# Optimization experiments

Hardware: AMD Instinct MI355X
Metric: run time of the kernel (lower is better)

## Reference

```python
import jax, jax.numpy as jnp
import numpy as np

B, S, IN_DIM = 8, 4096, 1024
H, D = 16, 64          # num_heads, head_dim (attention_dim = H*D = 1024)
OUT_DIM = 1024
EPS = 1e-6
HI = jax.lax.Precision.HIGHEST


def setup_inputs() -> dict:
    key = jax.random.key(0)
    ks = jax.random.split(key, 9)
    sx = 1.0 / np.sqrt(IN_DIM)
    so = 1.0 / np.sqrt(H * D)
    return {
        "x":  jax.random.normal(ks[0], (B, S, IN_DIM), jnp.float32),
        "wq": jax.random.normal(ks[1], (IN_DIM, H, D), jnp.float32) * sx,
        "bq": jnp.zeros((H, D), jnp.float32),
        "wk": jax.random.normal(ks[2], (IN_DIM, H, D), jnp.float32) * sx,
        "bk": jnp.zeros((H, D), jnp.float32),
        "wv": jax.random.normal(ks[3], (IN_DIM, H, D), jnp.float32) * sx,
        "bv": jnp.zeros((H, D), jnp.float32),
        "wo": jax.random.normal(ks[4], (H, D, OUT_DIM), jnp.float32) * so,
        "bo": jnp.zeros((OUT_DIM,), jnp.float32),
    }


def _feature_map(t):
    return jax.nn.elu(t) + 1.0


def reference(x, wq, bq, wk, bk, wv, bv, wo, bo):
    # QKV projections: [B,S,IN] x [IN,H,D] -> [B,S,H,D]
    q = jnp.einsum('bsi,ihd->bshd', x, wq) + bq
    k = jnp.einsum('bsi,ihd->bshd', x, wk) + bk
    v = jnp.einsum('bsi,ihd->bshd', x, wv) + bv

    Q = _feature_map(q)
    K = _feature_map(k)

    # Faithful to source: KV is an elementwise K*V reduced over seq -> [B,H,D]
    KV = jnp.einsum('bshd,bshd->bhd', K, v, precision=HI)
    Ksum = jnp.sum(K, axis=1)                      # [B,H,D]
    Z = 1.0 / (Q * Ksum[:, None, :, :] + EPS)      # [B,S,H,D]
    attn = Q * KV[:, None, :, :] * Z               # [B,S,H,D]

    # output projection contracts heads and head_dim
    out = jnp.einsum('bshd,hdo->bso', attn, wo) + bo
    return jax.nn.gelu(out)  # flax default gelu is approximate=True
```

## Files before the change

kernel.cpp:

```cpp
#include <hip/hip_runtime.h>


#define SEQ   4096
#define MROWS 32768
#define KDIM  1024
#define HD    1024
#define T32   32

typedef __bf16 bf16x8 __attribute__((ext_vector_type(8)));
typedef float floatx4 __attribute__((ext_vector_type(4)));

__device__ __forceinline__ unsigned short f2bf(float f) {
    unsigned int u = __float_as_uint(f);
    u += 0x7fffu + ((u >> 16) & 1u);
    return (unsigned short)(u >> 16);
}
__device__ __forceinline__ void cvt8(const float* __restrict__ p, unsigned short* d) {
    const float4 a = *(const float4*)p;
    const float4 b = *(const float4*)(p + 4);
    d[0] = f2bf(a.x); d[1] = f2bf(a.y); d[2] = f2bf(a.z); d[3] = f2bf(a.w);
    d[4] = f2bf(b.x); d[5] = f2bf(b.y); d[6] = f2bf(b.z); d[7] = f2bf(b.w);
}

typedef const __attribute__((address_space(1))) unsigned int* gas_t;
typedef __attribute__((address_space(3))) unsigned int* las_t;
__device__ __forceinline__ void async16(const void* g, void* l) {
    __builtin_amdgcn_global_load_lds((gas_t)g, (las_t)l, 16, 0, 0);
}

__global__ __launch_bounds__(256)
void prep(const float* __restrict__ x, unsigned short* __restrict__ xb,
          const float* __restrict__ wk, const float* __restrict__ wv,
          unsigned short* __restrict__ wkT, unsigned short* __restrict__ wvT,
          float4* __restrict__ KVZ4)
{
    __shared__ alignas(16) unsigned short Ts[64][72];
    const int t = threadIdx.x;
    if (blockIdx.x < 16384) {
        const size_t p = ((size_t)blockIdx.x * 256 + t) * 8;
        union { uint4 u; unsigned short s[8]; } o;
        cvt8(x + p, o.s);
        *(uint4*)(xb + p) = o.u;
        return;
    }
    if (blockIdx.x >= 16384 + 512) {
#pragma unroll
        for (int i = 0; i < 16; ++i)
            KVZ4[t * 16 + i] = (float4){0.f, 0.f, 0.f, 0.f};
        return;
    }
    const int bid = blockIdx.x - 16384;
    const float* W = (bid >> 8) ? wv : wk;
    unsigned short* WT = (bid >> 8) ? wvT : wkT;
    const int k0 = (bid & 15) * 64, n0 = ((bid >> 4) & 15) * 64;
    const int r4 = (t >> 4) * 4, c4 = (t & 15) * 4;
#pragma unroll
    for (int i = 0; i < 4; i++) {
        const float4 f = *(const float4*)(W + (size_t)(k0 + r4 + i) * HD + n0 + c4);
        Ts[c4 + 0][r4 + i] = f2bf(f.x);
        Ts[c4 + 1][r4 + i] = f2bf(f.y);
        Ts[c4 + 2][r4 + i] = f2bf(f.z);
        Ts[c4 + 3][r4 + i] = f2bf(f.w);
    }
    __syncthreads();
    const int rr = t >> 3, cc = (t & 7) * 8;
#pragma unroll
    for (int h = 0; h < 2; h++)
        *(uint4*)(WT + (size_t)(n0 + rr + h * 32) * KDIM + k0 + cc) =
            *(const uint4*)&Ts[rr + h * 32][cc];
}

__global__ __launch_bounds__(512, 1)
void kv_gemm_fast(const unsigned short* __restrict__ xb,
                  const unsigned short* __restrict__ wkT,
                  const unsigned short* __restrict__ wvT,
                  const float* __restrict__ bk, const float* __restrict__ bv,
                  float2* __restrict__ KVZ)
{
    __shared__ alignas(16) unsigned short As[4][256 * 32];
    __shared__ alignas(16) unsigned short Bs[4][256 * 32];

    const int t = threadIdx.x;

    const int id = blockIdx.x;
    const int xcd = id & 7, o = id >> 3;
    const int mtile = xcd * 16 + (o >> 3);
    const int ntile = o & 7;
    const int m0 = mtile * 256;
    const int n0 = ntile * 128;
    const int b  = m0 >> 12;

    const int w = t >> 6, lane = t & 63;
    const int wm = w >> 1, wn = w & 1;
    const int lrow = lane & 15, quad = lane >> 4;

    const int usw = quad ^ ((lrow >> 1) & 3);

    const int srow  = t >> 2;
    const int usrc  = (t & 3) ^ ((t >> 3) & 3);
    const unsigned short* gA0 = xb  + (size_t)(m0 + srow) * KDIM + usrc * 8;
    const unsigned short* gA1 = gA0 + (size_t)128 * KDIM;
    const unsigned short* gBk = wkT + (size_t)(n0 + srow) * KDIM + usrc * 8;
    const unsigned short* gBv = wvT + (size_t)(n0 + srow) * KDIM + usrc * 8;

#define STAGE(c, tk) do {                                                     \
        const int ko_ = (tk) * 32;                                            \
        async16(gA0 + ko_, &As[c][(0 * 512 + t) * 8]);                        \
        async16(gA1 + ko_, &As[c][(1 * 512 + t) * 8]);                        \
        async16(gBk + ko_, &Bs[c][(0 * 512 + t) * 8]);                        \
        async16(gBv + ko_, &Bs[c][(1 * 512 + t) * 8]);                        \
    } while (0)

    STAGE(0, 0);
    STAGE(1, 1);
    STAGE(2, 2);

    floatx4 accK[4][4], accV[4][4];
#pragma unroll
    for (int i = 0; i < 4; i++)
#pragma unroll
        for (int j = 0; j < 4; j++) {
            accK[i][j] = (floatx4){0.f, 0.f, 0.f, 0.f};
            accV[i][j] = (floatx4){0.f, 0.f, 0.f, 0.f};
        }

    asm volatile("s_waitcnt vmcnt(8)" ::: "memory");
    __builtin_amdgcn_s_barrier();

    for (int tk = 0; tk < T32; ++tk) {
        const unsigned short* A = As[tk & 3];
        const unsigned short* B = Bs[tk & 3];

        bf16x8 af[4], bK[4], bV[4];
#pragma unroll
        for (int mi = 0; mi < 4; ++mi)
            af[mi] = *(const bf16x8*)&A[(wm * 64 + mi * 16 + lrow) * 32 + usw * 8];
#pragma unroll
        for (int ni = 0; ni < 4; ++ni) {
            const int br = wn * 64 + ni * 16 + lrow;
            bK[ni] = *(const bf16x8*)&B[ br        * 32 + usw * 8];
            bV[ni] = *(const bf16x8*)&B[(br + 128) * 32 + usw * 8];
        }

        __builtin_amdgcn_s_setprio(1);
#pragma unroll
        for (int mi = 0; mi < 4; ++mi)
#pragma unroll
            for (int ni = 0; ni < 4; ++ni) {
                accK[mi][ni] = __builtin_amdgcn_mfma_f32_16x16x32_bf16(
                    af[mi], bK[ni], accK[mi][ni], 0, 0, 0);
                accV[mi][ni] = __builtin_amdgcn_mfma_f32_16x16x32_bf16(
                    af[mi], bV[ni], accV[mi][ni], 0, 0, 0);
            }
        __builtin_amdgcn_s_setprio(0);

        if (tk + 3 < T32) {
            STAGE((tk + 3) & 3, tk + 3);
            asm volatile("s_waitcnt vmcnt(8)" ::: "memory");
        } else if (tk == T32 - 3) {
            asm volatile("s_waitcnt vmcnt(4)" ::: "memory");
        } else if (tk == T32 - 2) {
            asm volatile("s_waitcnt vmcnt(0)" ::: "memory");
        }
        __builtin_amdgcn_s_barrier();
    }
#undef STAGE

#pragma unroll
    for (int ni = 0; ni < 4; ++ni) {
        const int colw = n0 + wn * 64 + ni * 16 + lrow;
        const float bkf = bk[colw];
        const float bvf = bv[colw];
        float pKV = 0.f, pK = 0.f;
#pragma unroll
        for (int mi = 0; mi < 4; ++mi) {
#pragma unroll
            for (int r = 0; r < 4; ++r) {
                const float kk = accK[mi][ni][r] + bkf;
                const float K  = (kk > 0.f) ? (kk + 1.f) : __expf(kk);
                const float vv = accV[mi][ni][r] + bvf;
                pKV += K * vv;
                pK  += K;
            }
        }
        pKV += __shfl_xor(pKV, 16, 64);
        pKV += __shfl_xor(pKV, 32, 64);
        pK  += __shfl_xor(pK, 16, 64);
        pK  += __shfl_xor(pK, 32, 64);
        if (quad == 0) {
            atomicAdd(&KVZ[b * HD + colw].x, pKV);
            atomicAdd(&KVZ[b * HD + colw].y, pK);
        }
    }
}

__global__ __launch_bounds__(256)
void kv_gemm(const float* __restrict__ x,
             const float* __restrict__ wk, const float* __restrict__ bk,
             const float* __restrict__ wv, const float* __restrict__ bv,
             float2* __restrict__ KVZ)
{
    __shared__ alignas(16) unsigned short As [128][40];
    __shared__ alignas(16) unsigned short BsK[128][40];
    __shared__ alignas(16) unsigned short BsV[128][40];

    const int t = threadIdx.x;
    const int n0 = blockIdx.x * 128;
    const int m0 = blockIdx.y * 128;
    const int b  = m0 >> 12;

    const int wave = t >> 6, lane = t & 63;
    const int wm = wave >> 1, wn = wave & 1;
    const int lrow = lane & 15, quad = lane >> 4;

    floatx4 accK[4][4], accV[4][4];
#pragma unroll
    for (int i = 0; i < 4; i++)
#pragma unroll
        for (int j = 0; j < 4; j++) {
            accK[i][j] = (floatx4){0.f, 0.f, 0.f, 0.f};
            accV[i][j] = (floatx4){0.f, 0.f, 0.f, 0.f};
        }

    const int arow0 = t >> 2, akc = (t & 3) * 8;
    const int bk0 = t >> 4, bnc = (t & 15) * 8;

    for (int k0 = 0; k0 < KDIM; k0 += 32) {
        __syncthreads();
        {
            union { uint4 u; unsigned short s[8]; } ua, ub;
            cvt8(x + (size_t)(m0 + arow0) * KDIM + k0 + akc, ua.s);
            cvt8(x + (size_t)(m0 + arow0 + 64) * KDIM + k0 + akc, ub.s);
            *(uint4*)&As[arow0][akc] = ua.u;
            *(uint4*)&As[arow0 + 64][akc] = ub.u;
        }
        {
            unsigned short k0s[8], k1s[8], v0s[8], v1s[8];
            cvt8(wk + (size_t)(k0 + bk0) * HD + n0 + bnc, k0s);
            cvt8(wk + (size_t)(k0 + bk0 + 16) * HD + n0 + bnc, k1s);
            cvt8(wv + (size_t)(k0 + bk0) * HD + n0 + bnc, v0s);
            cvt8(wv + (size_t)(k0 + bk0 + 16) * HD + n0 + bnc, v1s);
#pragma unroll
            for (int j = 0; j < 8; j++) {
                BsK[bnc + j][bk0]      = k0s[j];
                BsK[bnc + j][bk0 + 16] = k1s[j];
                BsV[bnc + j][bk0]      = v0s[j];
                BsV[bnc + j][bk0 + 16] = v1s[j];
            }
        }
        __syncthreads();

        bf16x8 af[4], bfK[4], bfV[4];
#pragma unroll
        for (int mi = 0; mi < 4; mi++)
            af[mi] = *(const bf16x8*)&As[wm * 64 + mi * 16 + lrow][quad * 8];
#pragma unroll
        for (int ni = 0; ni < 4; ni++) {
            bfK[ni] = *(const bf16x8*)&BsK[wn * 64 + ni * 16 + lrow][quad * 8];
            bfV[ni] = *(const bf16x8*)&BsV[wn * 64 + ni * 16 + lrow][quad * 8];
        }
#pragma unroll
        for (int mi = 0; mi < 4; mi++)
#pragma unroll
            for (int ni = 0; ni < 4; ni++) {
                accK[mi][ni] = __builtin_amdgcn_mfma_f32_16x16x32_bf16(
                    af[mi], bfK[ni], accK[mi][ni], 0, 0, 0);
                accV[mi][ni] = __builtin_amdgcn_mfma_f32_16x16x32_bf16(
                    af[mi], bfV[ni], accV[mi][ni], 0, 0, 0);
            }
    }

#pragma unroll
    for (int ni = 0; ni < 4; ni++) {
        const int colw = n0 + wn * 64 + ni * 16 + lrow;
        const float bkf = bk[colw];
        const float bvf = bv[colw];
        float pKV = 0.f, pK = 0.f;
#pragma unroll
        for (int mi = 0; mi < 4; mi++) {
#pragma unroll
            for (int r = 0; r < 4; r++) {
                const float kk = accK[mi][ni][r] + bkf;
                const float K  = (kk > 0.f) ? (kk + 1.f) : __expf(kk);
                const float vv = accV[mi][ni][r] + bvf;
                pKV += K * vv;
                pK  += K;
            }
        }
        pKV += __shfl_xor(pKV, 16, 64);
        pKV += __shfl_xor(pKV, 32, 64);
        pK  += __shfl_xor(pK, 16, 64);
        pK  += __shfl_xor(pK, 32, 64);
        if (quad == 0) {
            atomicAdd(&KVZ[b * HD + colw].x, pKV);
            atomicAdd(&KVZ[b * HD + colw].y, pK);
        }
    }
}

__global__ __launch_bounds__(256)
void rowgemm_bcast(const float2* __restrict__ KVZ,
                   const float* __restrict__ wo, const float* __restrict__ bo,
                   float* __restrict__ out)
{
    __shared__ float a[1024];
    __shared__ float red[4][64];
    __shared__ float sval[64];
    const int t = threadIdx.x;
    const int b = blockIdx.x;
    const int o0 = blockIdx.y * 64;
    const int s0 = blockIdx.z * 512;

    for (int c = t; c < 1024; c += 256) {
        const float2 z = KVZ[b * HD + c];
        a[c] = z.x / z.y;
    }
    __syncthreads();

    const int cs = t >> 6, oi = t & 63;
    float p = 0.f;
    const int cbeg = cs * 256;
    for (int c = cbeg; c < cbeg + 256; ++c)
        p += a[c] * wo[(size_t)c * HD + o0 + oi];
    red[cs][oi] = p;
    __syncthreads();

    if (t < 64) {
        float v = red[0][t] + red[1][t] + red[2][t] + red[3][t] + bo[o0 + t];
        sval[t] = 0.5f * v *
            (1.f + tanhf(0.7978845608028654f * (v + 0.044715f * v * v * v)));
    }
    __syncthreads();

    const float4 sv4 = *(const float4*)&sval[(t & 15) * 4];
    for (int r = t >> 4; r < 512; r += 16)
        *(float4*)&out[((size_t)(b * SEQ + s0 + r)) * HD + o0 + (t & 15) * 4] = sv4;
}

__global__ __launch_bounds__(256)
void rowgemm(const float2* __restrict__ KVZ,
             const float* __restrict__ wo, const float* __restrict__ bo,
             float* __restrict__ rowf)
{
    __shared__ float a[1024];
    __shared__ float red[4][64];
    const int t = threadIdx.x;
    const int b = blockIdx.x;
    const int o0 = blockIdx.y * 64;

    for (int c = t; c < 1024; c += 256) {
        const float2 z = KVZ[b * HD + c];
        a[c] = z.x / z.y;
    }
    __syncthreads();

    const int cs = t >> 6, oi = t & 63;
    float p = 0.f;
    const int cbeg = cs * 256;
    for (int c = cbeg; c < cbeg + 256; ++c)
        p += a[c] * wo[(size_t)c * HD + o0 + oi];
    red[cs][oi] = p;
    __syncthreads();

    if (t < 64) {
        float v = red[0][t] + red[1][t] + red[2][t] + red[3][t] + bo[o0 + t];
        const float g = 0.5f * v *
            (1.f + tanhf(0.7978845608028654f * (v + 0.044715f * v * v * v)));
        rowf[b * HD + o0 + t] = g;
    }
}

__global__ __launch_bounds__(256)
void broadcast_rows(const float* __restrict__ rowf, float* __restrict__ out)
{
    const size_t idx = (size_t)blockIdx.x * 256 + threadIdx.x;
    const size_t p = idx * 4;
    const int row = (int)(p >> 10);
    const int b = row >> 12;
    const int col = (int)(p & 1023);
    *(float4*)(out + p) = *(const float4*)(rowf + b * HD + col);
}

extern "C" void kernel_launch(void* const* d_in, const int* in_sizes, int n_in,
                              void* d_out, int out_size, void* d_ws, size_t ws_size,
                              hipStream_t stream)
{
    const float* x  = (const float*)d_in[0];
    const float* wk = (const float*)d_in[3];
    const float* bk = (const float*)d_in[4];
    const float* wv = (const float*)d_in[5];
    const float* bv = (const float*)d_in[6];
    const float* wo = (const float*)d_in[7];
    const float* bo = (const float*)d_in[8];
    float* out = (float*)d_out;

    const size_t NEED = (size_t)72 * 1024 * 1024;
    if (ws_size >= NEED) {
        unsigned short* xb  = (unsigned short*)d_ws;
        unsigned short* wkT = (unsigned short*)((char*)d_ws + (67u << 20));
        unsigned short* wvT = (unsigned short*)((char*)d_ws + (69u << 20));
        float2* KVZ = (float2*)((char*)d_ws + (71u << 20));

        prep<<<dim3(16384 + 512 + 1), 256, 0, stream>>>(x, xb, wk, wv, wkT, wvT,
                                                        (float4*)KVZ);
        kv_gemm_fast<<<dim3(1024), 512, 0, stream>>>(xb, wkT, wvT, bk, bv, KVZ);
        rowgemm_bcast<<<dim3(8, 16, 8), 256, 0, stream>>>(KVZ, wo, bo, out);
    } else {
        float2* KVZ = (float2*)d_ws;
        float* rowf = (float*)((char*)d_ws + 65536);
        hipMemsetAsync(KVZ, 0, 8 * HD * sizeof(float2), stream);
        kv_gemm<<<dim3(8, 256), 256, 0, stream>>>(x, wk, bk, wv, bv, KVZ);
        rowgemm<<<dim3(8, 16), 256, 0, stream>>>(KVZ, wo, bo, rowf);
        broadcast_rows<<<dim3((MROWS * HD / 4) / 256), 256, 0, stream>>>(rowf, out);
    }
}
```

Before: 400.0 us.

## Restructure KV-projection GEMM main loop into ping-pong phases with split staging

Rewrites the K/V projection GEMM main loop as an unrolled-by-two schedule that splits each k-step into separate K and V MFMA phases, each bracketed by barriers. A and B tile loads are issued in separate halves between phases, and the last k-steps are peeled into an explicit epilogue. The aim is to interleave global prefetch, LDS reads and MFMA bursts across waves, in the style of a ping-pong schedule. It adds many more barriers per k-step, which could cost more in synchronisation than the overlap gains.

```diff
diff --git a/kernel.cpp b/kernel.cpp
--- a/kernel.cpp
+++ b/kernel.cpp
@@ -5,7 +5,6 @@
 #define MROWS 32768
 #define KDIM  1024
 #define HD    1024
-#define T32   32
 
 typedef __bf16 bf16x8 __attribute__((ext_vector_type(8)));
 typedef float floatx4 __attribute__((ext_vector_type(4)));
@@ -103,17 +102,46 @@
     const unsigned short* gBk = wkT + (size_t)(n0 + srow) * KDIM + usrc * 8;
     const unsigned short* gBv = wvT + (size_t)(n0 + srow) * KDIM + usrc * 8;
 
-#define STAGE(c, tk) do {                                                     \
+#define STAGE_A(c, tk) do {                                                   \
         const int ko_ = (tk) * 32;                                            \
         async16(gA0 + ko_, &As[c][(0 * 512 + t) * 8]);                        \
         async16(gA1 + ko_, &As[c][(1 * 512 + t) * 8]);                        \
+    } while (0)
+#define STAGE_B(c, tk) do {                                                   \
+        const int ko_ = (tk) * 32;                                            \
         async16(gBk + ko_, &Bs[c][(0 * 512 + t) * 8]);                        \
         async16(gBv + ko_, &Bs[c][(1 * 512 + t) * 8]);                        \
     } while (0)
-
-    STAGE(0, 0);
-    STAGE(1, 1);
-    STAGE(2, 2);
+#define READ_AF(Ap_) do { _Pragma("unroll")                                   \
+        for (int mi = 0; mi < 4; ++mi)                                        \
+            af[mi] = *(const bf16x8*)&Ap_[(wm * 64 + mi * 16 + lrow) * 32 + usw * 8]; \
+    } while (0)
+#define READ_BK(Bp_) do { _Pragma("unroll")                                   \
+        for (int ni = 0; ni < 4; ++ni)                                        \
+            bK[ni] = *(const bf16x8*)&Bp_[(wn * 64 + ni * 16 + lrow) * 32 + usw * 8]; \
+    } while (0)
+#define READ_BV(Bp_) do { _Pragma("unroll")                                   \
+        for (int ni = 0; ni < 4; ++ni)                                        \
+            bV[ni] = *(const bf16x8*)&Bp_[(128 + wn * 64 + ni * 16 + lrow) * 32 + usw * 8]; \
+    } while (0)
+#define MFMA_K do { __builtin_amdgcn_s_setprio(1); _Pragma("unroll")          \
+        for (int mi = 0; mi < 4; ++mi) _Pragma("unroll")                      \
+            for (int ni = 0; ni < 4; ++ni)                                    \
+                accK[mi][ni] = __builtin_amdgcn_mfma_f32_16x16x32_bf16(       \
+                    af[mi], bK[ni], accK[mi][ni], 0, 0, 0);                   \
+        __builtin_amdgcn_s_setprio(0); } while (0)
+#define MFMA_V do { __builtin_amdgcn_s_setprio(1); _Pragma("unroll")          \
+        for (int mi = 0; mi < 4; ++mi) _Pragma("unroll")                      \
+            for (int ni = 0; ni < 4; ++ni)                                    \
+                accV[mi][ni] = __builtin_amdgcn_mfma_f32_16x16x32_bf16(       \
+                    af[mi], bV[ni], accV[mi][ni], 0, 0, 0);                   \
+        __builtin_amdgcn_s_setprio(0); } while (0)
+#define BAR   __builtin_amdgcn_s_barrier()
+#define VM(n) asm volatile("s_waitcnt vmcnt(" #n ")" ::: "memory")
+
+    STAGE_A(0, 0); STAGE_B(0, 0);
+    STAGE_A(1, 1); STAGE_B(1, 1);
+    STAGE_A(2, 2); STAGE_B(2, 2);
 
     floatx4 accK[4][4], accV[4][4];
 #pragma unroll
@@ -124,47 +152,76 @@
             accV[i][j] = (floatx4){0.f, 0.f, 0.f, 0.f};
         }
 
-    asm volatile("s_waitcnt vmcnt(8)" ::: "memory");
-    __builtin_amdgcn_s_barrier();
-
-    for (int tk = 0; tk < T32; ++tk) {
-        const unsigned short* A = As[tk & 3];
-        const unsigned short* B = Bs[tk & 3];
-
-        bf16x8 af[4], bK[4], bV[4];
-#pragma unroll
-        for (int mi = 0; mi < 4; ++mi)
-            af[mi] = *(const bf16x8*)&A[(wm * 64 + mi * 16 + lrow) * 32 + usw * 8];
-#pragma unroll
-        for (int ni = 0; ni < 4; ++ni) {
-            const int br = wn * 64 + ni * 16 + lrow;
-            bK[ni] = *(const bf16x8*)&B[ br        * 32 + usw * 8];
-            bV[ni] = *(const bf16x8*)&B[(br + 128) * 32 + usw * 8];
-        }
-
-        __builtin_amdgcn_s_setprio(1);
-#pragma unroll
-        for (int mi = 0; mi < 4; ++mi)
-#pragma unroll
-            for (int ni = 0; ni < 4; ++ni) {
-                accK[mi][ni] = __builtin_amdgcn_mfma_f32_16x16x32_bf16(
-                    af[mi], bK[ni], accK[mi][ni], 0, 0, 0);
-                accV[mi][ni] = __builtin_amdgcn_mfma_f32_16x16x32_bf16(
-                    af[mi], bV[ni], accV[mi][ni], 0, 0, 0);
-            }
-        __builtin_amdgcn_s_setprio(0);
-
-        if (tk + 3 < T32) {
-            STAGE((tk + 3) & 3, tk + 3);
-            asm volatile("s_waitcnt vmcnt(8)" ::: "memory");
-        } else if (tk == T32 - 3) {
-            asm volatile("s_waitcnt vmcnt(4)" ::: "memory");
-        } else if (tk == T32 - 2) {
-            asm volatile("s_waitcnt vmcnt(0)" ::: "memory");
-        }
-        __builtin_amdgcn_s_barrier();
-    }
-#undef STAGE
+    VM(8);
+    BAR;
+
+    bf16x8 af[4], bK[4], bV[4];
+
+    for (int it = 0; it < 14; ++it) {
+        const int tk = it * 2;
+        const unsigned short* A0 = As[tk & 3];
+        const unsigned short* B0 = Bs[tk & 3];
+        const unsigned short* A1 = As[(tk + 1) & 3];
+        const unsigned short* B1 = Bs[(tk + 1) & 3];
+
+        READ_AF(A0); READ_BK(B0);
+        STAGE_A((tk + 3) & 3, tk + 3);
+        BAR; MFMA_K; BAR;
+        READ_BV(B0);
+        STAGE_B((tk + 3) & 3, tk + 3);
+        BAR; MFMA_V; BAR;
+        READ_AF(A1); READ_BK(B1);
+        STAGE_A((tk + 4) & 3, tk + 4);
+        BAR; MFMA_K; BAR;
+        READ_BV(B1);
+        STAGE_B((tk + 4) & 3, tk + 4);
+        VM(8);
+        BAR; MFMA_V; BAR;
+    }
+
+    {
+        const unsigned short* A0 = As[0];
+        const unsigned short* B0 = Bs[0];
+        const unsigned short* A1 = As[1];
+        const unsigned short* B1 = Bs[1];
+        READ_AF(A0); READ_BK(B0);
+        STAGE_A(3, 31);
+        BAR; MFMA_K; BAR;
+        READ_BV(B0);
+        STAGE_B(3, 31);
+        VM(8);
+        BAR; MFMA_V; BAR;
+        READ_AF(A1); READ_BK(B1);
+        BAR; MFMA_K; BAR;
+        READ_BV(B1);
+        VM(4);
+        BAR; MFMA_V; BAR;
+    }
+    {
+        const unsigned short* A0 = As[2];
+        const unsigned short* B0 = Bs[2];
+        const unsigned short* A1 = As[3];
+        const unsigned short* B1 = Bs[3];
+        READ_AF(A0); READ_BK(B0);
+        BAR; MFMA_K; BAR;
+        READ_BV(B0);
+        VM(0);
+        BAR; MFMA_V; BAR;
+        READ_AF(A1); READ_BK(B1);
+        BAR; MFMA_K; BAR;
+        READ_BV(B1);
+        MFMA_V;
+    }
+
+#undef STAGE_A
+#undef STAGE_B
+#undef READ_AF
+#undef READ_BK
+#undef READ_BV
+#undef MFMA_K
+#undef MFMA_V
+#undef BAR
+#undef VM
 
 #pragma unroll
     for (int ni = 0; ni < 4; ++ni) {
```

Result: no change. 395.7 us (-1.1%).
